# Performance work log

Measured on AMD Instinct MI355X. Metric: run time of the kernel, lower is better.

Reference implementation:

```python
import jax, jax.numpy as jnp
import numpy as np

EPS = 1e-5

def _patches(x, k, stride, pad):
    # x: [B, C, H, W] -> [B, L, C*k*k] with patch features ordered (c, kh, kw)
    # matching torch unfold / adder2d weight layout [Cout, Cin, kh, kw].
    B, C, H, W = x.shape
    xp = jnp.pad(x, ((0, 0), (0, 0), (pad, pad), (pad, pad)))
    Ho = (H + 2 * pad - k) // stride + 1
    Wo = (W + 2 * pad - k) // stride + 1
    cols = [xp[:, :, i:i + stride * Ho:stride, j:j + stride * Wo:stride]
            for i in range(k) for j in range(k)]
    p = jnp.stack(cols, axis=2)                      # [B, C, k*k, Ho, Wo]
    p = p.reshape(B, C * k * k, Ho * Wo)             # [B, K, L]
    return p.transpose(0, 2, 1), Ho, Wo              # [B, L, K]


def adder2d(x, w, stride, pad):
    # AdderNet layer: out[n,co,h,w] = -sum_{ci,kh,kw} |x_patch - w[co]|
    B = x.shape[0]
    Cout, Cin, k, _ = w.shape
    P, Ho, Wo = _patches(x, k, stride, pad)          # [B, L, K]
    Wf = w.reshape(Cout, Cin * k * k)                # [Cout, K]

    @jax.checkpoint
    def per_out(wrow):                               # wrow: [K]
        return -jnp.sum(jnp.abs(P - wrow), axis=-1)  # [B, L]

    out = jax.lax.map(per_out, Wf)                   # [Cout, B, L]
    return out.transpose(1, 0, 2).reshape(B, Cout, Ho, Wo)


def batchnorm(x, gamma, beta):
    # training-mode BatchNorm2d: batch statistics over (N, H, W)
    mu = jnp.mean(x, axis=(0, 2, 3), keepdims=True)
    var = jnp.var(x, axis=(0, 2, 3), keepdims=True)
    xn = (x - mu) * jax.lax.rsqrt(var + EPS)
    return xn * gamma[None, :, None, None] + beta[None, :, None, None]


def setup_inputs() -> dict:
    key = jax.random.key(0)
    kx, kw1, kw2 = jax.random.split(key, 3)
    B, C, H, W = 32, 64, 32, 32
    return {
        "x": jax.random.normal(kx, (B, C, H, W), dtype=jnp.float32),
        "w1": jax.random.normal(kw1, (C, C, 3, 3), dtype=jnp.float32),
        "g1": jnp.ones((C,), dtype=jnp.float32),
        "b1": jnp.zeros((C,), dtype=jnp.float32),
        "w2": jax.random.normal(kw2, (C, C, 3, 3), dtype=jnp.float32),
        "g2": jnp.ones((C,), dtype=jnp.float32),
        "b2": jnp.zeros((C,), dtype=jnp.float32),
    }


def reference(x, w1, g1, b1, w2, g2, b2):
    out = adder2d(x, w1, stride=1, pad=1)
    out = jax.nn.relu(batchnorm(out, g1, b1))
    out = adder2d(out, w2, stride=1, pad=1)
    out = batchnorm(out, g2, b2)
    return jax.nn.relu(out + x)
```

## Files before the change

### kernel.cpp

```cpp
#include <hip/hip_runtime.h>

#define CH    64
#define HWHW  1024
#define CHW   65536
#define NPIX  32768.0f
#define KDIM  576

#define QSCALE 524288.0f
#define QBIAS  4194304.5f
#define Q0     4194304u
#define QINV   1.9073486328125e-6f

__device__ __forceinline__ unsigned quantf(float x) {
  return (unsigned)fmaf(x, QSCALE, QBIAS);
}

__device__ __forceinline__ unsigned sad_acc(unsigned x, unsigned w, unsigned a) {
  unsigned d;
  asm("v_sad_u32 %0, %1, %2, %3" : "=v"(d) : "v"(x), "v"(w), "v"(a));
  return d;
}

__global__ __launch_bounds__(256) void prep_kernel(
    const float* __restrict__ w1, const float* __restrict__ w2,
    unsigned* __restrict__ wt1, unsigned* __restrict__ wt2,
    float* __restrict__ stats) {
  int i = blockIdx.x * 256 + threadIdx.x;
  if (i < 256) stats[i] = 0.0f;
  if (i < CH * KDIM) {
    int co = i / KDIM, k = i % KDIM;
    int dst = (co >> 2) * 2304 + k * 4 + (co & 3);
    wt1[dst] = quantf(w1[i]);
    wt2[dst] = quantf(w2[i]);
  }
}

__global__ __launch_bounds__(256, 4) void adder_kernel(
    const float* __restrict__ xin,
    const unsigned* __restrict__ wt,
    float* __restrict__ out,
    float* __restrict__ stats) {
  const int cog  = blockIdx.x;
  const int rg   = blockIdx.y;
  const int n    = blockIdx.z;
  const int tid  = threadIdx.x;
  const int lane = tid & 63;
  const int wv   = __builtin_amdgcn_readfirstlane(tid >> 6);
  const int co0  = cog * 4;
  const int r0   = lane >> 3;
  const int c0   = (lane & 7) * 4;

  __shared__ unsigned xs[2][4][10][40];
  __shared__ unsigned wl[2304];
  __shared__ unsigned red[64][17];
  const int XSHALF = 4 * 10 * 40;

  const int i0 = tid,       ws0 = i0 / 80, rem0 = i0 % 80;
  const int row0 = rem0 >> 3, c40 = rem0 & 7;
  const int hr0 = rg * 8 - 1 + row0;
  const int i1 = tid + 256, ws1 = i1 / 80, rem1 = i1 % 80;
  const int row1 = rem1 >> 3, c41 = rem1 & 7;
  const int hr1 = rg * 8 - 1 + row1;
  const bool val0 = (hr0 >= 0) && (hr0 < 32);
  const bool val1 = (tid < 64) && (hr1 >= 0) && (hr1 < 32);
  const float* g0 = xin + n * CHW + ws0 * 16 * HWHW + hr0 * 32 + c40 * 4;
  const float* g1 = xin + n * CHW + ws1 * 16 * HWHW + hr1 * 32 + c41 * 4;
  unsigned* l0 = &xs[0][ws0][row0][1 + c40 * 4];
  unsigned* l1 = &xs[0][ws1][row1][1 + c41 * 4];

  {
    const uint4* wsrc = (const uint4*)(wt + cog * 2304);
    uint4* wdst = (uint4*)wl;
    for (int i = tid; i < 576; i += 256) wdst[i] = wsrc[i];
  }
  float4 a0, a1;
  if (val0) a0 = *(const float4*)g0;
  if (val1) a1 = *(const float4*)g1;
  {
    unsigned* p = (unsigned*)xs;
    for (int i = tid; i < 2 * XSHALF; i += 256) p[i] = Q0;
  }
  __syncthreads();
  if (val0) { l0[0] = quantf(a0.x); l0[1] = quantf(a0.y); l0[2] = quantf(a0.z); l0[3] = quantf(a0.w); }
  if (val1) { l1[0] = quantf(a1.x); l1[1] = quantf(a1.y); l1[2] = quantf(a1.z); l1[3] = quantf(a1.w); }
  __syncthreads();

  unsigned wA[12], wB[12];
  auto LOADW = [&](unsigned* dst, int ph) {
    const uint4* wp = (const uint4*)(wl + ph * 12);
    uint4 a = wp[0], b = wp[1], c = wp[2];
    dst[0] = a.x; dst[1] = a.y; dst[2]  = a.z; dst[3]  = a.w;
    dst[4] = b.x; dst[5] = b.y; dst[6]  = b.z; dst[7]  = b.w;
    dst[8] = c.x; dst[9] = c.y; dst[10] = c.z; dst[11] = c.w;
  };

  unsigned acc[4][4];
#pragma unroll
  for (int co = 0; co < 4; ++co)
#pragma unroll
    for (int j = 0; j < 4; ++j) acc[co][j] = 0u;

  auto COMPUTE = [&](const unsigned* w, int bufsel, int kh) {
    const unsigned* rowp = &xs[bufsel][wv][r0 + kh][c0];
    uint4 x4 = *(const uint4*)rowp;
    uint2 x2 = *(const uint2*)(rowp + 4);
    unsigned xv[6] = {x4.x, x4.y, x4.z, x4.w, x2.x, x2.y};
#pragma unroll
    for (int kw = 0; kw < 3; ++kw)
#pragma unroll
      for (int co = 0; co < 4; ++co) {
        unsigned ww = w[kw * 4 + co];
        acc[co][0] = sad_acc(xv[kw + 0], ww, acc[co][0]);
        acc[co][1] = sad_acc(xv[kw + 1], ww, acc[co][1]);
        acc[co][2] = sad_acc(xv[kw + 2], ww, acc[co][2]);
        acc[co][3] = sad_acc(xv[kw + 3], ww, acc[co][3]);
      }
  };

  const int PB = wv * 48;
  LOADW(wA, PB);
  for (int ci = 0; ci < 16; ci += 2) {
    const int p = PB + ci * 3;
    float4 b0, b1;
    if (val0) b0 = *(const float4*)(g0 + (ci + 1) * HWHW);
    if (val1) b1 = *(const float4*)(g1 + (ci + 1) * HWHW);
    LOADW(wB, p + 1);
    COMPUTE(wA, 0, 0);
    LOADW(wA, p + 2);
    COMPUTE(wB, 0, 1);
    LOADW(wB, p + 3);
    COMPUTE(wA, 0, 2);
    if (val0) { unsigned* d = l0 + XSHALF; d[0] = quantf(b0.x); d[1] = quantf(b0.y); d[2] = quantf(b0.z); d[3] = quantf(b0.w); }
    if (val1) { unsigned* d = l1 + XSHALF; d[0] = quantf(b1.x); d[1] = quantf(b1.y); d[2] = quantf(b1.z); d[3] = quantf(b1.w); }
    __syncthreads();
    const bool more = (ci + 2) < 16;
    float4 e0, e1;
    if (more && val0) e0 = *(const float4*)(g0 + (ci + 2) * HWHW);
    if (more && val1) e1 = *(const float4*)(g1 + (ci + 2) * HWHW);
    LOADW(wA, p + 4);
    COMPUTE(wB, 1, 0);
    LOADW(wB, p + 5);
    COMPUTE(wA, 1, 1);
    { int pn = more ? p + 6 : PB; LOADW(wA, pn); }
    COMPUTE(wB, 1, 2);
    if (more && val0) { l0[0] = quantf(e0.x); l0[1] = quantf(e0.y); l0[2] = quantf(e0.z); l0[3] = quantf(e0.w); }
    if (more && val1) { l1[0] = quantf(e1.x); l1[1] = quantf(e1.y); l1[2] = quantf(e1.z); l1[3] = quantf(e1.w); }
    __syncthreads();
  }

  unsigned* af = &acc[0][0];
  for (int src = 1; src < 4; ++src) {
    if (wv == src) {
#pragma unroll
      for (int j = 0; j < 16; ++j) red[lane][j] = af[j];
    }
    __syncthreads();
    if (wv == 0) {
#pragma unroll
      for (int j = 0; j < 16; ++j) af[j] += red[lane][j];
    }
    __syncthreads();
  }

  if (wv == 0) {
    const int ob = n * CHW + (rg * 8 + r0) * 32 + c0;
#pragma unroll
    for (int co = 0; co < 4; ++co) {
      float t0 = -(float)acc[co][0] * QINV;
      float t1 = -(float)acc[co][1] * QINV;
      float t2 = -(float)acc[co][2] * QINV;
      float t3 = -(float)acc[co][3] * QINV;
      *(float4*)(out + ob + (co0 + co) * HWHW) = make_float4(t0, t1, t2, t3);
      float sm = t0 + t1 + t2 + t3;
      float sq = t0 * t0 + t1 * t1 + t2 * t2 + t3 * t3;
#pragma unroll
      for (int m = 1; m < 64; m <<= 1) {
        sm += __shfl_xor(sm, m);
        sq += __shfl_xor(sq, m);
      }
      if (lane == 0) {
        atomicAdd(stats + co0 + co, sm);
        atomicAdd(stats + 64 + co0 + co, sq);
      }
    }
  }
}

__global__ __launch_bounds__(256) void bnrelu_kernel(
    const float* __restrict__ A, const float* __restrict__ stats,
    const float* __restrict__ g, const float* __restrict__ b,
    float* __restrict__ B) {
  int i = blockIdx.x * 256 + threadIdx.x;
  int c = (i >> 8) & 63;
  float mu  = stats[c] * (1.0f / NPIX);
  float var = fmaf(-mu, mu, stats[64 + c] * (1.0f / NPIX));
  float rs  = rsqrtf(var + 1e-5f);
  float ga  = g[c] * rs;
  float be  = fmaf(-mu, ga, b[c]);
  float4 v = ((const float4*)A)[i];
  v.x = fmaxf(fmaf(v.x, ga, be), 0.0f);
  v.y = fmaxf(fmaf(v.y, ga, be), 0.0f);
  v.z = fmaxf(fmaf(v.z, ga, be), 0.0f);
  v.w = fmaxf(fmaf(v.w, ga, be), 0.0f);
  ((float4*)B)[i] = v;
}

__global__ __launch_bounds__(256) void final_kernel(
    const float* __restrict__ Cbuf, const float* __restrict__ stats,
    const float* __restrict__ g, const float* __restrict__ b,
    const float* __restrict__ xres, float* __restrict__ out) {
  int i = blockIdx.x * 256 + threadIdx.x;
  int c = (i >> 8) & 63;
  float mu  = stats[c] * (1.0f / NPIX);
  float var = fmaf(-mu, mu, stats[64 + c] * (1.0f / NPIX));
  float rs  = rsqrtf(var + 1e-5f);
  float ga  = g[c] * rs;
  float be  = fmaf(-mu, ga, b[c]);
  float4 v = ((const float4*)Cbuf)[i];
  float4 xr = ((const float4*)xres)[i];
  v.x = fmaxf(fmaf(v.x, ga, be) + xr.x, 0.0f);
  v.y = fmaxf(fmaf(v.y, ga, be) + xr.y, 0.0f);
  v.z = fmaxf(fmaf(v.z, ga, be) + xr.z, 0.0f);
  v.w = fmaxf(fmaf(v.w, ga, be) + xr.w, 0.0f);
  ((float4*)out)[i] = v;
}

extern "C" void kernel_launch(void* const* d_in, const int* in_sizes, int n_in,
                              void* d_out, int out_size, void* d_ws, size_t ws_size,
                              hipStream_t stream) {
  const float* x  = (const float*)d_in[0];
  const float* w1 = (const float*)d_in[1];
  const float* g1 = (const float*)d_in[2];
  const float* b1 = (const float*)d_in[3];
  const float* w2 = (const float*)d_in[4];
  const float* g2 = (const float*)d_in[5];
  const float* b2 = (const float*)d_in[6];
  float* outp = (float*)d_out;

  float* ws = (float*)d_ws;
  const size_t NEL = 2097152;
  float*    bufA  = ws;
  float*    bufB  = ws + NEL;
  unsigned* wt1   = (unsigned*)(ws + 2 * NEL);
  unsigned* wt2   = wt1 + CH * KDIM;
  float*    stats = (float*)(wt2 + CH * KDIM);

  prep_kernel<<<144, 256, 0, stream>>>(w1, w2, wt1, wt2, stats);

  dim3 agrid(16, 4, 32);
  adder_kernel<<<agrid, 256, 0, stream>>>(x, wt1, bufA, stats);
  bnrelu_kernel<<<2048, 256, 0, stream>>>(bufA, stats, g1, b1, bufB);
  adder_kernel<<<agrid, 256, 0, stream>>>(bufB, wt2, bufA, stats + 128);
  final_kernel<<<2048, 256, 0, stream>>>(bufA, stats + 128, g2, b2, x, outp);
}
```

Baseline: 159.0 us.

## Make adder input staging per-wave, replacing block barriers with wave barriers

Each wave now loads, quantizes and stores only its own 16-channel slice into a private single-buffered LDS tile. This lets the per-channel loop use wave barriers instead of block-wide __syncthreads. The LDS footprint shrinks: rows are 36 wide, the zero padding is read through an offset trick, and the reduction scratch is aliased onto the same array. The cross-wave reduction becomes one store/sync/sum pass, and launch bounds are raised to allow 6 blocks per CU. The aim is less barrier stalling and higher occupancy. In exchange, the explicit double-buffered software pipeline and the weight register prefetch are dropped.

```diff
diff --git a/kernel.cpp b/kernel.cpp
--- a/kernel.cpp
+++ b/kernel.cpp
@@ -35,7 +35,7 @@
   }
 }
 
-__global__ __launch_bounds__(256, 4) void adder_kernel(
+__global__ __launch_bounds__(256, 6) void adder_kernel(
     const float* __restrict__ xin,
     const unsigned* __restrict__ wt,
     float* __restrict__ out,
@@ -50,119 +50,99 @@
   const int r0   = lane >> 3;
   const int c0   = (lane & 7) * 4;
 
-  __shared__ unsigned xs[2][4][10][40];
-  __shared__ unsigned wl[2304];
-  __shared__ unsigned red[64][17];
-  const int XSHALF = 4 * 10 * 40;
-
-  const int i0 = tid,       ws0 = i0 / 80, rem0 = i0 % 80;
-  const int row0 = rem0 >> 3, c40 = rem0 & 7;
-  const int hr0 = rg * 8 - 1 + row0;
-  const int i1 = tid + 256, ws1 = i1 / 80, rem1 = i1 % 80;
-  const int row1 = rem1 >> 3, c41 = rem1 & 7;
-  const int hr1 = rg * 8 - 1 + row1;
-  const bool val0 = (hr0 >= 0) && (hr0 < 32);
-  const bool val1 = (tid < 64) && (hr1 >= 0) && (hr1 < 32);
-  const float* g0 = xin + n * CHW + ws0 * 16 * HWHW + hr0 * 32 + c40 * 4;
-  const float* g1 = xin + n * CHW + ws1 * 16 * HWHW + hr1 * 32 + c41 * 4;
-  unsigned* l0 = &xs[0][ws0][row0][1 + c40 * 4];
-  unsigned* l1 = &xs[0][ws1][row1][1 + c41 * 4];
-
+  __shared__ __align__(16) unsigned lds[3840];
+  unsigned* xsw = lds + wv * 360;
+  unsigned* wl  = lds + 1440;
+  unsigned* red = lds;
+
+  const int rowA = lane >> 3, c4A = lane & 7;
+  const int hrA  = rg * 8 - 1 + rowA;
+  const bool vA  = (hrA >= 0) && (hrA < 32);
+  const int rowB = (lane + 64) >> 3, c4B = lane & 7;
+  const int hrB  = rg * 8 - 1 + rowB;
+  const bool vB  = (lane < 16) && (hrB >= 0) && (hrB < 32);
+  const float* gbase = xin + n * CHW + (wv * 16) * HWHW;
+  const float* gA = gbase + hrA * 32 + c4A * 4;
+  const float* gB = gbase + hrB * 32 + c4B * 4;
+  unsigned* dA = xsw + rowA * 36 + c4A * 4;
+  unsigned* dB = xsw + rowB * 36 + c4B * 4;
+
+  float4 a0, a1;
+  if (vA) a0 = *(const float4*)gA;
+  if (vB) a1 = *(const float4*)gB;
   {
     const uint4* wsrc = (const uint4*)(wt + cog * 2304);
-    uint4* wdst = (uint4*)wl;
-    for (int i = tid; i < 576; i += 256) wdst[i] = wsrc[i];
-  }
-  float4 a0, a1;
-  if (val0) a0 = *(const float4*)g0;
-  if (val1) a1 = *(const float4*)g1;
-  {
-    unsigned* p = (unsigned*)xs;
-    for (int i = tid; i < 2 * XSHALF; i += 256) p[i] = Q0;
-  }
+    for (int i = tid; i < 576; i += 256) ((uint4*)wl)[i] = wsrc[i];
+  }
+  for (int i = lane; i < 360; i += 64) xsw[i] = Q0;
   __syncthreads();
-  if (val0) { l0[0] = quantf(a0.x); l0[1] = quantf(a0.y); l0[2] = quantf(a0.z); l0[3] = quantf(a0.w); }
-  if (val1) { l1[0] = quantf(a1.x); l1[1] = quantf(a1.y); l1[2] = quantf(a1.z); l1[3] = quantf(a1.w); }
+  if (vA) { uint4 q = {quantf(a0.x), quantf(a0.y), quantf(a0.z), quantf(a0.w)}; *(uint4*)dA = q; }
+  if (vB) { uint4 q = {quantf(a1.x), quantf(a1.y), quantf(a1.z), quantf(a1.w)}; *(uint4*)dB = q; }
+
+  unsigned acc[4][4];
+#pragma unroll
+  for (int co = 0; co < 4; ++co)
+#pragma unroll
+    for (int j = 0; j < 4; ++j) acc[co][j] = 0u;
+
+  const int off0 = c0 ? (c0 - 1) : 33;
+
+  for (int ci = 0; ci < 16; ++ci) {
+    const bool more = ci < 15;
+    float4 b0, b1;
+    if (more && vA) b0 = *(const float4*)(gA + (ci + 1) * HWHW);
+    if (more && vB) b1 = *(const float4*)(gB + (ci + 1) * HWHW);
+
+    const int ph = wv * 48 + ci * 3;
+#pragma unroll
+    for (int kh = 0; kh < 3; ++kh) {
+      const uint4* wp = (const uint4*)(wl + (ph + kh) * 12);
+      uint4 wa = wp[0], wb = wp[1], wc = wp[2];
+      unsigned w[12] = {wa.x, wa.y, wa.z, wa.w, wb.x, wb.y, wb.z, wb.w,
+                        wc.x, wc.y, wc.z, wc.w};
+      const unsigned* rp = xsw + (r0 + kh) * 36;
+      uint4 x4 = *(const uint4*)(rp + c0);
+      unsigned xl = rp[off0];
+      unsigned xr = rp[c0 + 4];
+      unsigned xv[6] = {xl, x4.x, x4.y, x4.z, x4.w, xr};
+#pragma unroll
+      for (int kw = 0; kw < 3; ++kw)
+#pragma unroll
+        for (int co = 0; co < 4; ++co) {
+          unsigned ww = w[kw * 4 + co];
+          acc[co][0] = sad_acc(xv[kw + 0], ww, acc[co][0]);
+          acc[co][1] = sad_acc(xv[kw + 1], ww, acc[co][1]);
+          acc[co][2] = sad_acc(xv[kw + 2], ww, acc[co][2]);
+          acc[co][3] = sad_acc(xv[kw + 3], ww, acc[co][3]);
+        }
+    }
+    __builtin_amdgcn_wave_barrier();
+    if (more && vA) { uint4 q = {quantf(b0.x), quantf(b0.y), quantf(b0.z), quantf(b0.w)}; *(uint4*)dA = q; }
+    if (more && vB) { uint4 q = {quantf(b1.x), quantf(b1.y), quantf(b1.z), quantf(b1.w)}; *(uint4*)dB = q; }
+    __builtin_amdgcn_wave_barrier();
+  }
+
   __syncthreads();
-
-  unsigned wA[12], wB[12];
-  auto LOADW = [&](unsigned* dst, int ph) {
-    const uint4* wp = (const uint4*)(wl + ph * 12);
-    uint4 a = wp[0], b = wp[1], c = wp[2];
-    dst[0] = a.x; dst[1] = a.y; dst[2]  = a.z; dst[3]  = a.w;
-    dst[4] = b.x; dst[5] = b.y; dst[6]  = b.z; dst[7]  = b.w;
-    dst[8] = c.x; dst[9] = c.y; dst[10] = c.z; dst[11] = c.w;
-  };
-
-  unsigned acc[4][4];
-#pragma unroll
-  for (int co = 0; co < 4; ++co)
-#pragma unroll
-    for (int j = 0; j < 4; ++j) acc[co][j] = 0u;
-
-  auto COMPUTE = [&](const unsigned* w, int bufsel, int kh) {
-    const unsigned* rowp = &xs[bufsel][wv][r0 + kh][c0];
-    uint4 x4 = *(const uint4*)rowp;
-    uint2 x2 = *(const uint2*)(rowp + 4);
-    unsigned xv[6] = {x4.x, x4.y, x4.z, x4.w, x2.x, x2.y};
-#pragma unroll
-    for (int kw = 0; kw < 3; ++kw)
+  if (wv != 0) {
+    unsigned* rp = red + (wv - 1) * 1280 + lane * 20;
+#pragma unroll
+    for (int co = 0; co < 4; ++co) {
+      uint4 q = {acc[co][0], acc[co][1], acc[co][2], acc[co][3]};
+      *(uint4*)(rp + co * 4) = q;
+    }
+  }
+  __syncthreads();
+
+  if (wv == 0) {
+#pragma unroll
+    for (int s = 0; s < 3; ++s) {
+      const unsigned* rp = red + s * 1280 + lane * 20;
 #pragma unroll
       for (int co = 0; co < 4; ++co) {
-        unsigned ww = w[kw * 4 + co];
-        acc[co][0] = sad_acc(xv[kw + 0], ww, acc[co][0]);
-        acc[co][1] = sad_acc(xv[kw + 1], ww, acc[co][1]);
-        acc[co][2] = sad_acc(xv[kw + 2], ww, acc[co][2]);
-        acc[co][3] = sad_acc(xv[kw + 3], ww, acc[co][3]);
+        uint4 q = *(const uint4*)(rp + co * 4);
+        acc[co][0] += q.x; acc[co][1] += q.y; acc[co][2] += q.z; acc[co][3] += q.w;
       }
-  };
-
-  const int PB = wv * 48;
-  LOADW(wA, PB);
-  for (int ci = 0; ci < 16; ci += 2) {
-    const int p = PB + ci * 3;
-    float4 b0, b1;
-    if (val0) b0 = *(const float4*)(g0 + (ci + 1) * HWHW);
-    if (val1) b1 = *(const float4*)(g1 + (ci + 1) * HWHW);
-    LOADW(wB, p + 1);
-    COMPUTE(wA, 0, 0);
-    LOADW(wA, p + 2);
-    COMPUTE(wB, 0, 1);
-    LOADW(wB, p + 3);
-    COMPUTE(wA, 0, 2);
-    if (val0) { unsigned* d = l0 + XSHALF; d[0] = quantf(b0.x); d[1] = quantf(b0.y); d[2] = quantf(b0.z); d[3] = quantf(b0.w); }
-    if (val1) { unsigned* d = l1 + XSHALF; d[0] = quantf(b1.x); d[1] = quantf(b1.y); d[2] = quantf(b1.z); d[3] = quantf(b1.w); }
-    __syncthreads();
-    const bool more = (ci + 2) < 16;
-    float4 e0, e1;
-    if (more && val0) e0 = *(const float4*)(g0 + (ci + 2) * HWHW);
-    if (more && val1) e1 = *(const float4*)(g1 + (ci + 2) * HWHW);
-    LOADW(wA, p + 4);
-    COMPUTE(wB, 1, 0);
-    LOADW(wB, p + 5);
-    COMPUTE(wA, 1, 1);
-    { int pn = more ? p + 6 : PB; LOADW(wA, pn); }
-    COMPUTE(wB, 1, 2);
-    if (more && val0) { l0[0] = quantf(e0.x); l0[1] = quantf(e0.y); l0[2] = quantf(e0.z); l0[3] = quantf(e0.w); }
-    if (more && val1) { l1[0] = quantf(e1.x); l1[1] = quantf(e1.y); l1[2] = quantf(e1.z); l1[3] = quantf(e1.w); }
-    __syncthreads();
-  }
-
-  unsigned* af = &acc[0][0];
-  for (int src = 1; src < 4; ++src) {
-    if (wv == src) {
-#pragma unroll
-      for (int j = 0; j < 16; ++j) red[lane][j] = af[j];
-    }
-    __syncthreads();
-    if (wv == 0) {
-#pragma unroll
-      for (int j = 0; j < 16; ++j) af[j] += red[lane][j];
-    }
-    __syncthreads();
-  }
-
-  if (wv == 0) {
+    }
     const int ob = n * CHW + (rg * 8 + r0) * 32 + c0;
 #pragma unroll
     for (int co = 0; co < 4; ++co) {
```

Result: no change. 157.5 us (-1.0%).
